# Kernel tuning notes

Hardware: AMD Instinct MI355X
Metric: run time of the kernel (lower is better)

## Reference

```python
import jax, jax.numpy as jnp
import numpy as np

T, B, D, H, F, E = 2048, 2, 1024, 16, 4096, 8
HD = D // H
EPS = 1.1920929e-07  # torch.finfo(float32).eps


def setup_inputs() -> dict:
    key = jax.random.key(0)
    ks = jax.random.split(key, 20)
    sc = D ** -0.5
    n = lambda k, shape, s: jax.random.normal(k, shape, jnp.float32) * s
    return {
        "x": jax.random.normal(ks[0], (T, B, D), jnp.float32),
        "Wq": n(ks[1], (D, D), sc), "bq": jnp.zeros((D,), jnp.float32),
        "Wk": n(ks[2], (D, D), sc), "bk": jnp.zeros((D,), jnp.float32),
        "Wv": n(ks[3], (D, D), sc), "bv": jnp.zeros((D,), jnp.float32),
        "Wo": n(ks[4], (D, D), sc), "bo": jnp.zeros((D,), jnp.float32),
        "ln1_g": jnp.ones((D,), jnp.float32), "ln1_b": jnp.zeros((D,), jnp.float32),
        "ln2_g": jnp.ones((D,), jnp.float32), "ln2_b": jnp.zeros((D,), jnp.float32),
        "wg": n(ks[5], (D, E), sc),
        "W1": n(ks[6], (E, D, F), sc), "b1": jnp.zeros((E, F), jnp.float32),
        "W2": n(ks[7], (E, F, D), F ** -0.5), "b2": jnp.zeros((E, D), jnp.float32),
    }


def layer_norm(x, g, b):
    m = jnp.mean(x, -1, keepdims=True)
    v = jnp.var(x, -1, keepdims=True)
    return (x - m) * jax.lax.rsqrt(v + 1e-5) * g + b


def attention(x, Wq, bq, Wk, bk, Wv, bv, Wo, bo):
    t, b, d = x.shape
    q = ((x @ Wq + bq) * (HD ** -0.5)).reshape(t, b, H, HD)
    k = (x @ Wk + bk).reshape(t, b, H, HD)
    v = (x @ Wv + bv).reshape(t, b, H, HD)
    a = jax.nn.softmax(jnp.einsum('tbhd,sbhd->bhts', q, k), axis=-1)
    o = jnp.einsum('bhts,sbhd->tbhd', a, v).reshape(t, b, d)
    return o @ Wo + bo


def moe(xf, wg, W1, b1, W2, b2):
    # xf: [S, D] tokens (batch-major order, matching x.transpose(0,1).reshape(-1,d))
    S = xf.shape[0]
    C = 2 * ((S + E - 1) // E)  # fairseq top2 train capacity
    logits = xf.astype(jnp.float32) @ wg.astype(jnp.float32)
    gates = jax.nn.softmax(logits, axis=-1)
    idx1 = jnp.argmax(gates, axis=-1)
    m1 = jax.nn.one_hot(idx1, E, dtype=jnp.int32)
    idx2 = jnp.argmax(jnp.where(m1 > 0, -jnp.inf, logits), axis=-1)
    m2 = jax.nn.one_hot(idx2, E, dtype=jnp.int32)
    g1 = jnp.take_along_axis(gates, idx1[:, None], 1)[:, 0]
    g2 = jnp.take_along_axis(gates, idx2[:, None], 1)[:, 0]
    loc1 = jnp.cumsum(m1, axis=0) - 1
    loc2 = jnp.cumsum(m2, axis=0) - 1 + jnp.sum(m1, axis=0, keepdims=True)
    pos1 = jnp.sum(loc1 * m1, axis=1)
    pos2 = jnp.sum(loc2 * m2, axis=1)
    l_aux = jnp.mean(jnp.mean(gates, 0) * jnp.mean(m1.astype(jnp.float32), 0)) * E * E
    k1 = (pos1 < C).astype(xf.dtype)
    k2 = (pos2 < C).astype(xf.dtype)
    g1 = g1.astype(xf.dtype) * k1
    g2 = g2.astype(xf.dtype) * k2
    den = jnp.maximum(g1 + g2, EPS)
    g1, g2 = g1 / den, g2 / den
    f1 = idx1 * C + jnp.minimum(pos1, C - 1)
    f2 = idx2 * C + jnp.minimum(pos2, C - 1)
    # dispatch (unweighted, capacity-masked)
    buf = jnp.zeros((E * C, D), xf.dtype)
    buf = buf.at[f1].add(xf * k1[:, None]).at[f2].add(xf * k2[:, None])
    h = jax.nn.relu(jnp.einsum('ecd,edf->ecf', buf.reshape(E, C, D), W1) + b1[:, None, :])
    out = (jnp.einsum('ecf,efd->ecd', h, W2) + b2[:, None, :]).reshape(E * C, D)
    # combine with normalized gates (dropped tokens have zero gate)
    y = g1[:, None] * out[f1] + g2[:, None] * out[f2]
    return y, l_aux


def reference(x, Wq, bq, Wk, bk, Wv, bv, Wo, bo, ln1_g, ln1_b, ln2_g, ln2_b, wg, W1, b1, W2, b2):
    # pre-LN self-attention block
    residual = x
    h = layer_norm(x, ln1_g, ln1_b)
    h = attention(h, Wq, bq, Wk, bk, Wv, bv, Wo, bo)
    x = residual + h
    # pre-LN MoE FFN block
    residual = x
    h = layer_norm(x, ln2_g, ln2_b)
    hb = jnp.swapaxes(h, 0, 1).reshape(-1, D)  # [B*T, D]
    y, l_aux = moe(hb, wg, W1, b1, W2, b2)
    y = jnp.swapaxes(y.reshape(B, T, D), 0, 1)
    x = residual + y
    return x, l_aux
```

## Files before the change

kernel.cpp:

```cpp
#include <hip/hip_runtime.h>

#define TT 2048
#define BB 2
#define DD 1024
#define HH 16
#define HD 64
#define FF 4096
#define EE 8
#define SS (TT*BB)
#define CAP 1024
#define EPSF 1.1920929e-07f

typedef __attribute__((ext_vector_type(8))) short short8;
typedef __attribute__((ext_vector_type(4))) float floatx4;

static __device__ inline unsigned short f2bf(float f){
    unsigned int u = __float_as_uint(f);
    unsigned int r = (u + 0x7fffu + ((u>>16)&1u)) >> 16;
    return (unsigned short)r;
}
static __device__ inline float bf2f(unsigned short h){
    return __uint_as_float(((unsigned int)h)<<16);
}
static __device__ inline void split2(float x, unsigned short& h, unsigned short& l){
    unsigned short hh = f2bf(x);
    h = hh;
    l = f2bf(x - bf2f(hh));
}
static __device__ inline void split2t(float x, unsigned short& h, unsigned short& l){
    unsigned int u = __float_as_uint(x);
    unsigned int hu = u & 0xffff0000u;
    h = (unsigned short)(hu>>16);
    float r = x - __uint_as_float(hu);
    l = (unsigned short)(__float_as_uint(r)>>16);
}
#define GETF4(v,j) ((j)==0?(v).x:(j)==1?(v).y:(j)==2?(v).z:(v).w)
#define GETU4(v,j) ((j)==0?(v).x:(j)==1?(v).y:(j)==2?(v).z:(v).w)

__global__ __launch_bounds__(256) void ln_kernel(const float* __restrict__ x,
    const float* __restrict__ gam, const float* __restrict__ bet, float* __restrict__ o)
{
    int row = blockIdx.x;
    int tid = threadIdx.x;
    float4 v = ((const float4*)(x + (size_t)row*DD))[tid];
    float s  = v.x+v.y+v.z+v.w;
    float ss = v.x*v.x+v.y*v.y+v.z*v.z+v.w*v.w;
    __shared__ float r1[256], r2[256];
    r1[tid]=s; r2[tid]=ss;
    __syncthreads();
    for (int off=128; off>0; off>>=1){
        if (tid<off){ r1[tid]+=r1[tid+off]; r2[tid]+=r2[tid+off]; }
        __syncthreads();
    }
    float mean = r1[0] * (1.f/DD);
    float var  = r2[0] * (1.f/DD) - mean*mean;
    float inv  = 1.f / sqrtf(var + 1e-5f);
    float4 g = ((const float4*)gam)[tid];
    float4 b = ((const float4*)bet)[tid];
    float4 r;
    r.x = (v.x-mean)*inv*g.x + b.x;
    r.y = (v.y-mean)*inv*g.y + b.y;
    r.z = (v.z-mean)*inv*g.z + b.z;
    r.w = (v.w-mean)*inv*g.w + b.w;
    ((float4*)(o + (size_t)row*DD))[tid] = r;
}

__global__ __launch_bounds__(256) void ln_split_kernel(const float* __restrict__ x,
    const float* __restrict__ gam, const float* __restrict__ bet,
    unsigned short* __restrict__ oh, unsigned short* __restrict__ ol)
{
    int row = blockIdx.x;
    int tid = threadIdx.x;
    float4 v = ((const float4*)(x + (size_t)row*DD))[tid];
    float s  = v.x+v.y+v.z+v.w;
    float ss = v.x*v.x+v.y*v.y+v.z*v.z+v.w*v.w;
    __shared__ float r1[256], r2[256];
    r1[tid]=s; r2[tid]=ss;
    __syncthreads();
    for (int off=128; off>0; off>>=1){
        if (tid<off){ r1[tid]+=r1[tid+off]; r2[tid]+=r2[tid+off]; }
        __syncthreads();
    }
    float mean = r1[0] * (1.f/DD);
    float var  = r2[0] * (1.f/DD) - mean*mean;
    float inv  = 1.f / sqrtf(var + 1e-5f);
    float4 g = ((const float4*)gam)[tid];
    float4 b = ((const float4*)bet)[tid];
    float4 r;
    r.x = (v.x-mean)*inv*g.x + b.x;
    r.y = (v.y-mean)*inv*g.y + b.y;
    r.z = (v.z-mean)*inv*g.z + b.z;
    r.w = (v.w-mean)*inv*g.w + b.w;
    ushort4 hv, lv;
    split2(r.x, hv.x, lv.x);
    split2(r.y, hv.y, lv.y);
    split2(r.z, hv.z, lv.z);
    split2(r.w, hv.w, lv.w);
    ((ushort4*)(oh + (size_t)row*DD))[tid] = hv;
    ((ushort4*)(ol + (size_t)row*DD))[tid] = lv;
}

template<bool RELU, bool OUTBF16>
__global__ __launch_bounds__(256) void gemm_mfma(
    const unsigned short* __restrict__ A, const unsigned short* __restrict__ Bt,
    const float* __restrict__ bias, float* __restrict__ Cf,
    unsigned short* __restrict__ Cb,
    int M, int N, int K, long wStride, int bStride, int rowsPerExp)
{
    __shared__ unsigned short As[128*64];
    __shared__ unsigned short Bs[128*64];
    const int tid = threadIdx.x, lane = tid&63;
    const int w = tid>>6, wr = w>>1, wc = w&1;
    const int m0 = blockIdx.y*128, n0 = blockIdx.x*128;
    const int e = m0 / rowsPerExp;
    const unsigned short* Bp = Bt + (size_t)e*wStride;
    const int srow = tid>>3, sslot = tid&7;
    floatx4 zf = {0.f,0.f,0.f,0.f};
    floatx4 acc[4][4];
    #pragma unroll
    for (int m=0;m<4;m++)
        #pragma unroll
        for (int n=0;n<4;n++) acc[m][n]=zf;

    short8 ar[4], br[4];
    #pragma unroll
    for (int i=0;i<4;i++){
        int r = srow + i*32;
        ar[i] = *(const short8*)(A  + (size_t)(m0+r)*K + sslot*8);
        br[i] = *(const short8*)(Bp + (size_t)(n0+r)*K + sslot*8);
    }
    const int NT = K/64;
    for (int kt=0; kt<NT; kt++){
        __syncthreads();
        #pragma unroll
        for (int i=0;i<4;i++){
            int r = srow + i*32;
            int off = r*64 + ((sslot ^ (r&7))<<3);
            *(short8*)(&As[off]) = ar[i];
            *(short8*)(&Bs[off]) = br[i];
        }
        __syncthreads();
        if (kt+1 < NT){
            int k0 = (kt+1)*64;
            #pragma unroll
            for (int i=0;i<4;i++){
                int r = srow + i*32;
                ar[i] = *(const short8*)(A  + (size_t)(m0+r)*K + k0 + sslot*8);
                br[i] = *(const short8*)(Bp + (size_t)(n0+r)*K + k0 + sslot*8);
            }
        }
        #pragma unroll
        for (int kk=0;kk<2;kk++){
            short8 af[4], bf[4];
            int kgrp = kk*4 + (lane>>4);
            #pragma unroll
            for (int m=0;m<4;m++){
                int rowa = wr*64 + m*16 + (lane&15);
                af[m] = *(const short8*)(&As[rowa*64 + ((kgrp ^ (rowa&7))<<3)]);
                int rowb = wc*64 + m*16 + (lane&15);
                bf[m] = *(const short8*)(&Bs[rowb*64 + ((kgrp ^ (rowb&7))<<3)]);
            }
            #pragma unroll
            for (int m=0;m<4;m++)
                #pragma unroll
                for (int n=0;n<4;n++)
                    acc[m][n] = __builtin_amdgcn_mfma_f32_16x16x32_bf16(af[m], bf[n], acc[m][n], 0,0,0);
        }
    }
    int colg = n0 + wc*64 + (lane&15);
    int rowg = m0 + wr*64 + ((lane>>4)<<2);
    #pragma unroll
    for (int n=0;n<4;n++){
        float bv = bias[e*bStride + colg + n*16];
        #pragma unroll
        for (int m=0;m<4;m++){
            #pragma unroll
            for (int i2=0;i2<4;i2++){
                float v = acc[m][n][i2] + bv;
                if (RELU) v = fmaxf(v, 0.f);
                size_t o = (size_t)(rowg + m*16 + i2)*N + colg + n*16;
                if (OUTBF16) Cb[o] = f2bf(v); else Cf[o] = v;
            }
        }
    }
}

template<bool QKV>
__global__ __launch_bounds__(256) void gemm_mfma_s(
    const unsigned short* __restrict__ Ahi, const unsigned short* __restrict__ Alo,
    const unsigned short* __restrict__ Bhi, const unsigned short* __restrict__ Blo,
    const float* __restrict__ b0, const float* __restrict__ b1p, const float* __restrict__ b2p,
    const float* __restrict__ res,
    float* __restrict__ o0,
    unsigned short* __restrict__ kh, unsigned short* __restrict__ kl,
    unsigned short* __restrict__ vh, unsigned short* __restrict__ vl,
    int M, int K)
{
    __shared__ unsigned short As[128*64];
    __shared__ unsigned short Bs[128*64];
    const int tid = threadIdx.x, lane = tid&63;
    const int w = tid>>6, wr = w>>1, wc = w&1;
    const int m0 = blockIdx.y*128, n0 = blockIdx.x*128;
    const int row = tid>>1, khalf = tid&1;
    floatx4 zf = {0.f,0.f,0.f,0.f};
    floatx4 acc[4][4];
    #pragma unroll
    for (int m=0;m<4;m++)
        #pragma unroll
        for (int n=0;n<4;n++) acc[m][n]=zf;

    short8 awh0,awh1,awl0,awl1, bwh0,bwh1,bwl0,bwl1;
    {
        size_t ao = (size_t)(m0+row)*K + khalf*16;
        awh0 = *(const short8*)(Ahi+ao); awh1 = *(const short8*)(Ahi+ao+8);
        awl0 = *(const short8*)(Alo+ao); awl1 = *(const short8*)(Alo+ao+8);
        size_t bo = (size_t)(n0+row)*K + khalf*16;
        bwh0 = *(const short8*)(Bhi+bo); bwh1 = *(const short8*)(Bhi+bo+8);
        bwl0 = *(const short8*)(Blo+bo); bwl1 = *(const short8*)(Blo+bo+8);
    }
    const int NT = K/32;
    for (int kt=0; kt<NT; kt++){
        __syncthreads();
        {
            int base = row*64, sw = row&7;
            int g0 = khalf*2, g1 = khalf*2+1;
            *(short8*)(&As[base + ((g0^sw)<<3)])     = awh0;
            *(short8*)(&As[base + ((g1^sw)<<3)])     = awh1;
            *(short8*)(&As[base + (((g0+4)^sw)<<3)]) = awl0;
            *(short8*)(&As[base + (((g1+4)^sw)<<3)]) = awl1;
            *(short8*)(&Bs[base + ((g0^sw)<<3)])     = bwh0;
            *(short8*)(&Bs[base + ((g1^sw)<<3)])     = bwh1;
            *(short8*)(&Bs[base + (((g0+4)^sw)<<3)]) = bwl0;
            *(short8*)(&Bs[base + (((g1+4)^sw)<<3)]) = bwl1;
        }
        __syncthreads();
        if (kt+1 < NT){
            int k0 = (kt+1)*32;
            size_t ao = (size_t)(m0+row)*K + k0 + khalf*16;
            awh0 = *(const short8*)(Ahi+ao); awh1 = *(const short8*)(Ahi+ao+8);
            awl0 = *(const short8*)(Alo+ao); awl1 = *(const short8*)(Alo+ao+8);
            size_t bo = (size_t)(n0+row)*K + k0 + khalf*16;
            bwh0 = *(const short8*)(Bhi+bo); bwh1 = *(const short8*)(Bhi+bo+8);
            bwl0 = *(const short8*)(Blo+bo); bwl1 = *(const short8*)(Blo+bo+8);
        }
        {
            int kg = lane>>4;
            short8 afh[4], afl[4], bfh[4], bfl[4];
            #pragma unroll
            for (int m=0;m<4;m++){
                int ra = wr*64 + m*16 + (lane&15);
                afh[m] = *(const short8*)(&As[ra*64 + ((kg ^ (ra&7))<<3)]);
                afl[m] = *(const short8*)(&As[ra*64 + (((kg+4) ^ (ra&7))<<3)]);
                int rb = wc*64 + m*16 + (lane&15);
                bfh[m] = *(const short8*)(&Bs[rb*64 + ((kg ^ (rb&7))<<3)]);
                bfl[m] = *(const short8*)(&Bs[rb*64 + (((kg+4) ^ (rb&7))<<3)]);
            }
            #pragma unroll
            for (int m=0;m<4;m++)
                #pragma unroll
                for (int n=0;n<4;n++){
                    acc[m][n] = __builtin_amdgcn_mfma_f32_16x16x32_bf16(afl[m], bfh[n], acc[m][n], 0,0,0);
                    acc[m][n] = __builtin_amdgcn_mfma_f32_16x16x32_bf16(afh[m], bfl[n], acc[m][n], 0,0,0);
                    acc[m][n] = __builtin_amdgcn_mfma_f32_16x16x32_bf16(afh[m], bfh[n], acc[m][n], 0,0,0);
                }
        }
    }
    int colg = n0 + wc*64 + (lane&15);
    int rowg = m0 + wr*64 + ((lane>>4)<<2);
    if (QKV){
        int chunk = n0>>10;
        int colc = colg & 1023;
        const float* bp = chunk==0 ? b0 : (chunk==1 ? b1p : b2p);
        #pragma unroll
        for (int n=0;n<4;n++){
            float bv = bp[colc + n*16];
            #pragma unroll
            for (int m=0;m<4;m++){
                #pragma unroll
                for (int i2=0;i2<4;i2++){
                    int r = rowg + m*16 + i2;
                    float v = acc[m][n][i2] + bv;
                    size_t off = (size_t)r*DD + colc + n*16;
                    if (chunk==0){
                        o0[off] = v*0.125f;
                    } else {
                        unsigned short hh, ll;
                        split2(v, hh, ll);
                        if (chunk==1){ kh[off]=hh; kl[off]=ll; }
                        else         { vh[off]=hh; vl[off]=ll; }
                    }
                }
            }
        }
    } else {
        #pragma unroll
        for (int n=0;n<4;n++){
            float bv = b0[colg + n*16];
            #pragma unroll
            for (int m=0;m<4;m++){
                #pragma unroll
                for (int i2=0;i2<4;i2++){
                    int r = rowg + m*16 + i2;
                    float v = acc[m][n][i2] + bv + res[(size_t)r*DD + colg + n*16];
                    o0[(size_t)r*DD + colg + n*16] = v;
                }
            }
        }
    }
}

__global__ __launch_bounds__(256) void attn_mfma(const float* __restrict__ q,
    const unsigned short* __restrict__ khi, const unsigned short* __restrict__ klo,
    const unsigned short* __restrict__ vhi, const unsigned short* __restrict__ vlo,
    unsigned short* __restrict__ ohi, unsigned short* __restrict__ olo)
{
    __shared__ unsigned short Kh[64*64], Kl[64*64];
    __shared__ unsigned short Vh[64*64], Vl[64*64];
    __shared__ unsigned short Ph[4*16*64];
    const int tid = threadIdx.x, lane = tid&63, w = tid>>6;
    const int t0 = blockIdx.x*64;
    const int b = blockIdx.y>>4, h = blockIdx.y&15;

    short8 qh[2], ql[2];
    #pragma unroll
    for (int kk=0;kk<2;kk++){
        const float* qp = q + ((size_t)(t0 + 16*w + (lane&15))*BB + b)*DD + h*64 + kk*32 + (lane>>4)*8;
        float4 f0 = ((const float4*)qp)[0];
        float4 f1 = ((const float4*)qp)[1];
        unsigned short hh[8], ll[8];
        #pragma unroll
        for (int j=0;j<4;j++){ split2(GETF4(f0,j), hh[j], ll[j]); }
        #pragma unroll
        for (int j=0;j<4;j++){ split2(GETF4(f1,j), hh[4+j], ll[4+j]); }
        qh[kk] = *(short8*)hh; ql[kk] = *(short8*)ll;
    }

    const int kr = tid>>2, kq = tid&3;
    const int vs0 = (tid&15)*4, vd0 = (tid>>4)*4;
    short8 kwh0,kwh1,kwl0,kwl1;
    ushort4 vwh[4], vwl[4];
    {
        const unsigned short* kp = khi + ((size_t)kr*BB + b)*DD + h*64 + kq*16;
        const unsigned short* lp = klo + ((size_t)kr*BB + b)*DD + h*64 + kq*16;
        kwh0 = *(const short8*)(kp); kwh1 = *(const short8*)(kp+8);
        kwl0 = *(const short8*)(lp); kwl1 = *(const short8*)(lp+8);
        #pragma unroll
        for (int i=0;i<4;i++){
            size_t vo = ((size_t)(vs0+i)*BB + b)*DD + h*64 + vd0;
            vwh[i] = *(const ushort4*)(vhi + vo);
            vwl[i] = *(const ushort4*)(vlo + vo);
        }
    }

    float m_st[4] = {-3.0e38f,-3.0e38f,-3.0e38f,-3.0e38f};
    float l_st[4] = {0.f,0.f,0.f,0.f};
    floatx4 zf = {0.f,0.f,0.f,0.f};
    floatx4 oacc[4];
    #pragma unroll
    for (int n=0;n<4;n++) oacc[n]=zf;

    for (int s0=0; s0<TT; s0+=64){
        __syncthreads();
        {
            int base = kr*64, sw = kr&7;
            int g0 = kq*2, g1 = kq*2+1;
            *(short8*)(&Kh[base + ((g0^sw)<<3)]) = kwh0;
            *(short8*)(&Kh[base + ((g1^sw)<<3)]) = kwh1;
            *(short8*)(&Kl[base + ((g0^sw)<<3)]) = kwl0;
            *(short8*)(&Kl[base + ((g1^sw)<<3)]) = kwl1;
        }
        {
            int g = vs0>>3, so = vs0&7;
            #pragma unroll
            for (int j=0;j<4;j++){
                int d = vd0 + j;
                ushort4 hv, lv;
                hv.x=GETU4(vwh[0],j); hv.y=GETU4(vwh[1],j); hv.z=GETU4(vwh[2],j); hv.w=GETU4(vwh[3],j);
                lv.x=GETU4(vwl[0],j); lv.y=GETU4(vwl[1],j); lv.z=GETU4(vwl[2],j); lv.w=GETU4(vwl[3],j);
                int off = d*64 + ((g ^ (d&7))<<3) + so;
                *(ushort4*)(&Vh[off]) = hv;
                *(ushort4*)(&Vl[off]) = lv;
            }
        }
        __syncthreads();
        if (s0+64 < TT){
            const unsigned short* kp = khi + ((size_t)(s0+64+kr)*BB + b)*DD + h*64 + kq*16;
            const unsigned short* lp = klo + ((size_t)(s0+64+kr)*BB + b)*DD + h*64 + kq*16;
            kwh0 = *(const short8*)(kp); kwh1 = *(const short8*)(kp+8);
            kwl0 = *(const short8*)(lp); kwl1 = *(const short8*)(lp+8);
            #pragma unroll
            for (int i=0;i<4;i++){
                size_t vo = ((size_t)(s0+64+vs0+i)*BB + b)*DD + h*64 + vd0;
                vwh[i] = *(const ushort4*)(vhi + vo);
                vwl[i] = *(const ushort4*)(vlo + vo);
            }
        }
        floatx4 sacc[4];
        __builtin_amdgcn_s_setprio(1);
        #pragma unroll
        for (int n=0;n<4;n++){
            floatx4 s = zf;
            #pragma unroll
            for (int kk=0;kk<2;kk++){
                int g = kk*4 + (lane>>4);
                int rb = n*16 + (lane&15);
                short8 kbh = *(const short8*)(&Kh[rb*64 + ((g ^ (rb&7))<<3)]);
                short8 kbl = *(const short8*)(&Kl[rb*64 + ((g ^ (rb&7))<<3)]);
                s = __builtin_amdgcn_mfma_f32_16x16x32_bf16(ql[kk], kbh, s, 0,0,0);
                s = __builtin_amdgcn_mfma_f32_16x16x32_bf16(qh[kk], kbl, s, 0,0,0);
                s = __builtin_amdgcn_mfma_f32_16x16x32_bf16(qh[kk], kbh, s, 0,0,0);
            }
            sacc[n] = s;
        }
        __builtin_amdgcn_s_setprio(0);
        float mx[4];
        #pragma unroll
        for (int r=0;r<4;r++)
            mx[r] = fmaxf(fmaxf(sacc[0][r], sacc[1][r]), fmaxf(sacc[2][r], sacc[3][r]));
        #pragma unroll
        for (int sh=1; sh<16; sh<<=1){
            #pragma unroll
            for (int r=0;r<4;r++) mx[r] = fmaxf(mx[r], __shfl_xor(mx[r], sh));
        }
        float corr[4];
        #pragma unroll
        for (int r=0;r<4;r++){
            float nm = fmaxf(m_st[r], mx[r]);
            corr[r] = __expf(m_st[r] - nm);
            m_st[r] = nm;
        }
        float ts[4] = {0.f,0.f,0.f,0.f};
        #pragma unroll
        for (int n=0;n<4;n++){
            #pragma unroll
            for (int r=0;r<4;r++){
                float p = __expf(sacc[n][r] - m_st[r]);
                ts[r] += p;
                int q2 = ((lane>>4)<<2) + r;
                int s2 = n*16 + (lane&15);
                int off = w*1024 + q2*64 + (((s2>>3) ^ (q2&7))<<3) + (s2&7);
                Ph[off] = f2bf(p);
            }
        }
        #pragma unroll
        for (int sh=1; sh<16; sh<<=1){
            #pragma unroll
            for (int r=0;r<4;r++) ts[r] += __shfl_xor(ts[r], sh);
        }
        #pragma unroll
        for (int r=0;r<4;r++) l_st[r] = l_st[r]*corr[r] + ts[r];
        #pragma unroll
        for (int n=0;n<4;n++)
            #pragma unroll
            for (int r=0;r<4;r++) oacc[n][r] *= corr[r];
        __builtin_amdgcn_s_setprio(1);
        #pragma unroll
        for (int kk=0;kk<2;kk++){
            int g = kk*4 + (lane>>4);
            int rq = lane&15;
            short8 pa = *(const short8*)(&Ph[w*1024 + rq*64 + ((g ^ (rq&7))<<3)]);
            #pragma unroll
            for (int n=0;n<4;n++){
                int rd = n*16 + (lane&15);
                short8 vbh = *(const short8*)(&Vh[rd*64 + ((g ^ (rd&7))<<3)]);
                short8 vbl = *(const short8*)(&Vl[rd*64 + ((g ^ (rd&7))<<3)]);
                oacc[n] = __builtin_amdgcn_mfma_f32_16x16x32_bf16(pa, vbl, oacc[n], 0,0,0);
                oacc[n] = __builtin_amdgcn_mfma_f32_16x16x32_bf16(pa, vbh, oacc[n], 0,0,0);
            }
        }
        __builtin_amdgcn_s_setprio(0);
    }
    float il[4];
    #pragma unroll
    for (int r=0;r<4;r++) il[r] = 1.f/l_st[r];
    int qrow = t0 + 16*w + ((lane>>4)<<2);
    #pragma unroll
    for (int n=0;n<4;n++){
        #pragma unroll
        for (int r=0;r<4;r++){
            float v = oacc[n][r]*il[r];
            unsigned short hh, ll;
            split2(v, hh, ll);
            size_t off = ((size_t)(qrow+r)*BB + b)*DD + h*64 + n*16 + (lane&15);
            ohi[off] = hh; olo[off] = ll;
        }
    }
}

__global__ __launch_bounds__(256) void transpose_bf16_k(const float* __restrict__ in,
    unsigned short* __restrict__ outp, int R, int C)
{
    __shared__ float t[64][65];
    int e = blockIdx.z;
    const float* ip = in + (size_t)e*R*C;
    unsigned short* op = outp + (size_t)e*R*C;
    int r0 = blockIdx.y*64, c0 = blockIdx.x*64;
    int tid = threadIdx.x;
    #pragma unroll
    for (int i=0;i<4;i++){
        int ch = i*256 + tid;
        int r = ch>>4, c4 = (ch&15)*4;
        float4 v = *(const float4*)(ip + (size_t)(r0+r)*C + c0 + c4);
        t[r][c4+0]=v.x; t[r][c4+1]=v.y; t[r][c4+2]=v.z; t[r][c4+3]=v.w;
    }
    __syncthreads();
    #pragma unroll
    for (int i=0;i<4;i++){
        int ch = i*256 + tid;
        int rr = ch>>4, c4 = (ch&15)*4;
        ushort4 o;
        o.x = f2bf(t[c4+0][rr]); o.y = f2bf(t[c4+1][rr]);
        o.z = f2bf(t[c4+2][rr]); o.w = f2bf(t[c4+3][rr]);
        *(ushort4*)(op + (size_t)(c0+rr)*R + r0 + c4) = o;
    }
}

__global__ __launch_bounds__(256) void transpose_split_k(const float* __restrict__ in,
    unsigned short* __restrict__ oh, unsigned short* __restrict__ ol, int R, int C)
{
    __shared__ float t[64][65];
    int r0 = blockIdx.y*64, c0 = blockIdx.x*64;
    int tid = threadIdx.x;
    #pragma unroll
    for (int i=0;i<4;i++){
        int ch = i*256 + tid;
        int r = ch>>4, c4 = (ch&15)*4;
        float4 v = *(const float4*)(in + (size_t)(r0+r)*C + c0 + c4);
        t[r][c4+0]=v.x; t[r][c4+1]=v.y; t[r][c4+2]=v.z; t[r][c4+3]=v.w;
    }
    __syncthreads();
    #pragma unroll
    for (int i=0;i<4;i++){
        int ch = i*256 + tid;
        int rr = ch>>4, c4 = (ch&15)*4;
        ushort4 hv, lv;
        split2(t[c4+0][rr], hv.x, lv.x);
        split2(t[c4+1][rr], hv.y, lv.y);
        split2(t[c4+2][rr], hv.z, lv.z);
        split2(t[c4+3][rr], hv.w, lv.w);
        size_t off = (size_t)(c0+rr)*R + r0 + c4;
        *(ushort4*)(oh + off) = hv;
        *(ushort4*)(ol + off) = lv;
    }
}

__global__ __launch_bounds__(256) void gather_bf16_k(const float* __restrict__ h2,
    const int* __restrict__ s2r, unsigned short* __restrict__ buf)
{
    int s = blockIdx.x; int row = s2r[s]; int c = threadIdx.x;
    float4 v = make_float4(0.f,0.f,0.f,0.f);
    if (row>=0) v = *(const float4*)(h2 + (size_t)row*DD + c*4);
    ushort4 o;
    o.x=f2bf(v.x); o.y=f2bf(v.y); o.z=f2bf(v.z); o.w=f2bf(v.w);
    *(ushort4*)(buf + (size_t)s*DD + c*4) = o;
}

__global__ __launch_bounds__(256) void route_kernel(const float* __restrict__ h2,
    const float* __restrict__ wgm, float* __restrict__ gates,
    int* __restrict__ idx1, int* __restrict__ idx2,
    float* __restrict__ g1, float* __restrict__ g2)
{
    int wid = threadIdx.x >> 6, lane = threadIdx.x & 63;
    int s = blockIdx.x*4 + wid;
    int row = (s % TT)*BB + (s / TT);
    const float* hr = h2 + (size_t)row*DD;
    float acc[EE] = {};
    #pragma unroll
    for (int c=0;c<16;c++){
        int d = c*64 + lane;
        float xv = hr[d];
        const float* wr = wgm + (size_t)d*EE;
        #pragma unroll
        for (int e2=0;e2<EE;e2++) acc[e2] += xv * wr[e2];
    }
    #pragma unroll
    for (int off=32; off>0; off>>=1){
        #pragma unroll
        for (int e2=0;e2<EE;e2++) acc[e2] += __shfl_down(acc[e2], off);
    }
    if (lane==0){
        float mx = acc[0];
        #pragma unroll
        for (int e2=1;e2<EE;e2++) mx = fmaxf(mx, acc[e2]);
        float ex[EE]; float sum=0.f;
        #pragma unroll
        for (int e2=0;e2<EE;e2++){ ex[e2] = __expf(acc[e2]-mx); sum += ex[e2]; }
        float inv = 1.f/sum;
        int i1=0; float bv1=acc[0];
        #pragma unroll
        for (int e2=1;e2<EE;e2++){ if (acc[e2] > bv1){ bv1=acc[e2]; i1=e2; } }
        int i2=-1; float bv2=-3.0e38f;
        #pragma unroll
        for (int e2=0;e2<EE;e2++){ if (e2!=i1 && acc[e2] > bv2){ bv2=acc[e2]; i2=e2; } }
        #pragma unroll
        for (int e2=0;e2<EE;e2++) gates[(size_t)s*EE + e2] = ex[e2]*inv;
        idx1[s]=i1; idx2[s]=i2;
        g1[s]=ex[i1]*inv; g2[s]=ex[i2]*inv;
    }
}

__global__ __launch_bounds__(256) void scan_kernel(
    const float* __restrict__ gates, const int* __restrict__ idx1, const int* __restrict__ idx2,
    const float* __restrict__ g1, const float* __restrict__ g2,
    float* __restrict__ g1n, float* __restrict__ g2n,
    int* __restrict__ f1, int* __restrict__ f2, int* __restrict__ slot2row,
    float* __restrict__ laux)
{
    __shared__ int i1s[SS];
    __shared__ int i2s[SS];
    __shared__ int cnt1[256][EE];
    __shared__ int cnt2[256][EE];
    __shared__ float gsum[256][EE];
    __shared__ int tot1[EE];
    int tid = threadIdx.x;
    for (int i=tid;i<EE*CAP;i+=256) slot2row[i] = -1;
    for (int i=tid;i<SS;i+=256){ i1s[i]=idx1[i]; i2s[i]=idx2[i]; }
    __syncthreads();
    int c1l[EE]={}, c2l[EE]={};
    float gl[EE]={};
    int base = tid*16;
    for (int qq=0;qq<16;qq++){
        int s = base+qq;
        c1l[i1s[s]]++; c2l[i2s[s]]++;
        #pragma unroll
        for (int e2=0;e2<EE;e2++) gl[e2] += gates[(size_t)s*EE+e2];
    }
    #pragma unroll
    for (int e2=0;e2<EE;e2++){ cnt1[tid][e2]=c1l[e2]; cnt2[tid][e2]=c2l[e2]; gsum[tid][e2]=gl[e2]; }
    __syncthreads();
    if (tid < EE){
        int e2 = tid;
        int run=0;
        for (int t=0;t<256;t++){ int tmp=cnt1[t][e2]; cnt1[t][e2]=run; run+=tmp; }
        tot1[e2]=run;
        run=0;
        for (int t=0;t<256;t++){ int tmp=cnt2[t][e2]; cnt2[t][e2]=run; run+=tmp; }
        float gr=0.f;
        for (int t=0;t<256;t++) gr += gsum[t][e2];
        gsum[0][e2]=gr;
    }
    __syncthreads();
    int p1[EE], p2[EE];
    #pragma unroll
    for (int e2=0;e2<EE;e2++){ p1[e2]=cnt1[tid][e2]; p2[e2]=cnt2[tid][e2]+tot1[e2]; }
    for (int qq=0;qq<16;qq++){
        int s = base+qq;
        int e1 = i1s[s], e2v = i2s[s];
        int pos1 = p1[e1]++;
        int pos2 = p2[e2v]++;
        float gv1 = g1[s], gv2 = g2[s];
        float gm1 = (pos1<CAP)? gv1 : 0.f;
        float gm2 = (pos2<CAP)? gv2 : 0.f;
        float den = fmaxf(gm1+gm2, EPSF);
        g1n[s] = gm1/den; g2n[s] = gm2/den;
        int ff1 = e1*CAP + (pos1<CAP?pos1:CAP-1);
        int ff2 = e2v*CAP + (pos2<CAP?pos2:CAP-1);
        f1[s]=ff1; f2[s]=ff2;
        int hrow = (s % TT)*BB + (s / TT);
        if (pos1<CAP) slot2row[ff1]=hrow;
        if (pos2<CAP) slot2row[ff2]=hrow;
    }
    if (tid==0){
        float a=0.f;
        #pragma unroll
        for (int e2=0;e2<EE;e2++) a += (gsum[0][e2]*(1.f/SS)) * ((float)tot1[e2]*(1.f/SS));
        laux[0] = a * (float)EE;
    }
}

__global__ __launch_bounds__(256) void combine_kernel(const float* __restrict__ x2,
    const float* __restrict__ eout, const float* __restrict__ g1n, const float* __restrict__ g2n,
    const int* __restrict__ f1, const int* __restrict__ f2, float* __restrict__ out)
{
    int s = blockIdx.x;
    float a = g1n[s], b = g2n[s];
    int s1 = f1[s], s2 = f2[s];
    int row = (s % TT)*BB + (s / TT);
    int c = threadIdx.x;
    float4 o1 = ((const float4*)(eout + (size_t)s1*DD))[c];
    float4 o2 = ((const float4*)(eout + (size_t)s2*DD))[c];
    float4 xr = ((const float4*)(x2 + (size_t)row*DD))[c];
    float4 r;
    r.x = xr.x + a*o1.x + b*o2.x;
    r.y = xr.y + a*o1.y + b*o2.y;
    r.z = xr.z + a*o1.z + b*o2.z;
    r.w = xr.w + a*o1.w + b*o2.w;
    ((float4*)(out + (size_t)row*DD))[c] = r;
}

extern "C" void kernel_launch(void* const* d_in, const int* in_sizes, int n_in,
                              void* d_out, int out_size, void* d_ws, size_t ws_size,
                              hipStream_t stream)
{
    const float* x    = (const float*)d_in[0];
    const float* Wq   = (const float*)d_in[1];
    const float* bq   = (const float*)d_in[2];
    const float* Wk   = (const float*)d_in[3];
    const float* bk   = (const float*)d_in[4];
    const float* Wv   = (const float*)d_in[5];
    const float* bv   = (const float*)d_in[6];
    const float* Wo   = (const float*)d_in[7];
    const float* bo   = (const float*)d_in[8];
    const float* ln1g = (const float*)d_in[9];
    const float* ln1b = (const float*)d_in[10];
    const float* ln2g = (const float*)d_in[11];
    const float* ln2b = (const float*)d_in[12];
    const float* wgm  = (const float*)d_in[13];
    const float* W1   = (const float*)d_in[14];
    const float* b1   = (const float*)d_in[15];
    const float* W2   = (const float*)d_in[16];
    const float* b2   = (const float*)d_in[17];
    float* out = (float*)d_out;

    char* w = (char*)d_ws;
    unsigned short* h1hi = (unsigned short*)(w);
    unsigned short* h1lo = (unsigned short*)(w + ((size_t)8<<20));
    float*          qb   = (float*)(w + ((size_t)16<<20));
    unsigned short* Khg  = (unsigned short*)(w + ((size_t)32<<20));
    unsigned short* Klg  = (unsigned short*)(w + ((size_t)40<<20));
    unsigned short* Vhg  = (unsigned short*)(w + ((size_t)48<<20));
    unsigned short* Vlg  = (unsigned short*)(w + ((size_t)56<<20));
    float*          x2   = (float*)(w + ((size_t)64<<20));
    unsigned short* bufb = (unsigned short*)(w + ((size_t)80<<20));
    unsigned short* hb   = (unsigned short*)(w + ((size_t)96<<20));
    unsigned short* Bqkv_hi = (unsigned short*)(w + ((size_t)96<<20));
    unsigned short* Bqkv_lo = (unsigned short*)(w + ((size_t)102<<20));
    unsigned short* Bo_hi   = (unsigned short*)(w + ((size_t)108<<20));
    unsigned short* Bo_lo   = (unsigned short*)(w + ((size_t)110<<20));
    unsigned short* W1t  = (unsigned short*)(w + ((size_t)160<<20));
    unsigned short* W2t  = (unsigned short*)(w + ((size_t)224<<20));
    float*          ffno = (float*)(w + ((size_t)32<<20));
    char*  sm   = w + ((size_t)288<<20);
    float* gates   = (float*)(sm);                sm += (size_t)SS*EE*4;
    int*   idx1    = (int*)(sm);                  sm += SS*4;
    int*   idx2    = (int*)(sm);                  sm += SS*4;
    float* g1      = (float*)(sm);                sm += SS*4;
    float* g2      = (float*)(sm);                sm += SS*4;
    float* g1n     = (float*)(sm);                sm += SS*4;
    float* g2n     = (float*)(sm);                sm += SS*4;
    int*   f1      = (int*)(sm);                  sm += SS*4;
    int*   f2      = (int*)(sm);                  sm += SS*4;
    int*   slot2row= (int*)(sm);                  sm += EE*CAP*4;

    transpose_bf16_k<<<dim3(FF/64, DD/64, EE), 256, 0, stream>>>(W1, W1t, DD, FF);
    transpose_bf16_k<<<dim3(DD/64, FF/64, EE), 256, 0, stream>>>(W2, W2t, FF, DD);
    transpose_split_k<<<dim3(16,16), 256, 0, stream>>>(Wq, Bqkv_hi,                   Bqkv_lo,                   DD, DD);
    transpose_split_k<<<dim3(16,16), 256, 0, stream>>>(Wk, Bqkv_hi + (size_t)DD*DD,   Bqkv_lo + (size_t)DD*DD,   DD, DD);
    transpose_split_k<<<dim3(16,16), 256, 0, stream>>>(Wv, Bqkv_hi + (size_t)2*DD*DD, Bqkv_lo + (size_t)2*DD*DD, DD, DD);
    transpose_split_k<<<dim3(16,16), 256, 0, stream>>>(Wo, Bo_hi, Bo_lo, DD, DD);
    ln_split_kernel<<<SS, 256, 0, stream>>>(x, ln1g, ln1b, h1hi, h1lo);
    gemm_mfma_s<true><<<dim3(24, SS/128), 256, 0, stream>>>(
        h1hi, h1lo, Bqkv_hi, Bqkv_lo, bq, bk, bv, nullptr, qb, Khg, Klg, Vhg, Vlg, SS, DD);
    attn_mfma<<<dim3(TT/64, BB*HH), 256, 0, stream>>>(qb, Khg, Klg, Vhg, Vlg, h1hi, h1lo);
    gemm_mfma_s<false><<<dim3(8, SS/128), 256, 0, stream>>>(
        h1hi, h1lo, Bo_hi, Bo_lo, bo, bo, bo, x, x2, nullptr, nullptr, nullptr, nullptr, SS, DD);
    ln_kernel<<<SS, 256, 0, stream>>>(x2, ln2g, ln2b, qb);
    route_kernel<<<SS/4, 256, 0, stream>>>(qb, wgm, gates, idx1, idx2, g1, g2);
    scan_kernel<<<1, 256, 0, stream>>>(gates, idx1, idx2, g1, g2,
        g1n, g2n, f1, f2, slot2row, out + (size_t)SS*DD);
    gather_bf16_k<<<EE*CAP, 256, 0, stream>>>(qb, slot2row, bufb);
    gemm_mfma<true,true><<<dim3(FF/128, (EE*CAP)/128), 256, 0, stream>>>(
        bufb, W1t, b1, nullptr, hb, EE*CAP, FF, DD, (long)FF*DD, FF, CAP);
    gemm_mfma<false,false><<<dim3(DD/128, (EE*CAP)/128), 256, 0, stream>>>(
        hb, W2t, b2, ffno, nullptr, EE*CAP, DD, FF, (long)DD*FF, DD, CAP);
    combine_kernel<<<SS, 256, 0, stream>>>(x2, ffno, g1n, g2n, f1, f2, out);
    (void)in_sizes; (void)n_in; (void)out_size; (void)ws_size;
}
```

Baseline: 673.0 us.

## Double attention query tile to 128 rows with 512-thread blocks sharing K/V tiles

The attention kernel now processes 128 query rows per block with 8 waves instead of 64 rows with 4 waves. Each K/V tile staged in shared memory is reused by twice as many queries, which halves global K/V traffic. The cooperative load mapping is reworked so each of the 512 threads loads half as much. The trade-off is half as many blocks (512) on the GPU and larger per-block shared memory for P, which may reduce occupancy and parallelism.

```diff
diff --git a/kernel.cpp b/kernel.cpp
--- a/kernel.cpp
+++ b/kernel.cpp
@@ -26,13 +26,6 @@
     unsigned short hh = f2bf(x);
     h = hh;
     l = f2bf(x - bf2f(hh));
-}
-static __device__ inline void split2t(float x, unsigned short& h, unsigned short& l){
-    unsigned int u = __float_as_uint(x);
-    unsigned int hu = u & 0xffff0000u;
-    h = (unsigned short)(hu>>16);
-    float r = x - __uint_as_float(hu);
-    l = (unsigned short)(__float_as_uint(r)>>16);
 }
 #define GETF4(v,j) ((j)==0?(v).x:(j)==1?(v).y:(j)==2?(v).z:(v).w)
 #define GETU4(v,j) ((j)==0?(v).x:(j)==1?(v).y:(j)==2?(v).z:(v).w)
@@ -309,16 +302,16 @@
     }
 }
 
-__global__ __launch_bounds__(256) void attn_mfma(const float* __restrict__ q,
+__global__ __launch_bounds__(512) void attn_mfma(const float* __restrict__ q,
     const unsigned short* __restrict__ khi, const unsigned short* __restrict__ klo,
     const unsigned short* __restrict__ vhi, const unsigned short* __restrict__ vlo,
     unsigned short* __restrict__ ohi, unsigned short* __restrict__ olo)
 {
     __shared__ unsigned short Kh[64*64], Kl[64*64];
     __shared__ unsigned short Vh[64*64], Vl[64*64];
-    __shared__ unsigned short Ph[4*16*64];
+    __shared__ unsigned short Ph[8*16*64];
     const int tid = threadIdx.x, lane = tid&63, w = tid>>6;
-    const int t0 = blockIdx.x*64;
+    const int t0 = blockIdx.x*128;
     const int b = blockIdx.y>>4, h = blockIdx.y&15;
 
     short8 qh[2], ql[2];
@@ -335,17 +328,16 @@
         qh[kk] = *(short8*)hh; ql[kk] = *(short8*)ll;
     }
 
-    const int kr = tid>>2, kq = tid&3;
-    const int vs0 = (tid&15)*4, vd0 = (tid>>4)*4;
-    short8 kwh0,kwh1,kwl0,kwl1;
-    ushort4 vwh[4], vwl[4];
+    const int kr = tid>>3, kq = tid&7;
+    const int vs0 = (tid&31)*2, vd0 = (tid>>5)*4;
+    short8 kwh, kwl;
+    ushort4 vwh[2], vwl[2];
     {
-        const unsigned short* kp = khi + ((size_t)kr*BB + b)*DD + h*64 + kq*16;
-        const unsigned short* lp = klo + ((size_t)kr*BB + b)*DD + h*64 + kq*16;
-        kwh0 = *(const short8*)(kp); kwh1 = *(const short8*)(kp+8);
-        kwl0 = *(const short8*)(lp); kwl1 = *(const short8*)(lp+8);
-        #pragma unroll
-        for (int i=0;i<4;i++){
+        size_t ko = ((size_t)kr*BB + b)*DD + h*64 + kq*8;
+        kwh = *(const short8*)(khi + ko);
+        kwl = *(const short8*)(klo + ko);
+        #pragma unroll
+        for (int i=0;i<2;i++){
             size_t vo = ((size_t)(vs0+i)*BB + b)*DD + h*64 + vd0;
             vwh[i] = *(const ushort4*)(vhi + vo);
             vwl[i] = *(const ushort4*)(vlo + vo);
@@ -362,34 +354,30 @@
     for (int s0=0; s0<TT; s0+=64){
         __syncthreads();
         {
-            int base = kr*64, sw = kr&7;
-            int g0 = kq*2, g1 = kq*2+1;
-            *(short8*)(&Kh[base + ((g0^sw)<<3)]) = kwh0;
-            *(short8*)(&Kh[base + ((g1^sw)<<3)]) = kwh1;
-            *(short8*)(&Kl[base + ((g0^sw)<<3)]) = kwl0;
-            *(short8*)(&Kl[base + ((g1^sw)<<3)]) = kwl1;
+            int off = kr*64 + ((kq ^ (kr&7))<<3);
+            *(short8*)(&Kh[off]) = kwh;
+            *(short8*)(&Kl[off]) = kwl;
         }
         {
             int g = vs0>>3, so = vs0&7;
             #pragma unroll
             for (int j=0;j<4;j++){
                 int d = vd0 + j;
-                ushort4 hv, lv;
-                hv.x=GETU4(vwh[0],j); hv.y=GETU4(vwh[1],j); hv.z=GETU4(vwh[2],j); hv.w=GETU4(vwh[3],j);
-                lv.x=GETU4(vwl[0],j); lv.y=GETU4(vwl[1],j); lv.z=GETU4(vwl[2],j); lv.w=GETU4(vwl[3],j);
+                ushort2 hv, lv;
+                hv.x=GETU4(vwh[0],j); hv.y=GETU4(vwh[1],j);
+                lv.x=GETU4(vwl[0],j); lv.y=GETU4(vwl[1],j);
                 int off = d*64 + ((g ^ (d&7))<<3) + so;
-                *(ushort4*)(&Vh[off]) = hv;
-                *(ushort4*)(&Vl[off]) = lv;
+                *(ushort2*)(&Vh[off]) = hv;
+                *(ushort2*)(&Vl[off]) = lv;
             }
         }
         __syncthreads();
         if (s0+64 < TT){
-            const unsigned short* kp = khi + ((size_t)(s0+64+kr)*BB + b)*DD + h*64 + kq*16;
-            const unsigned short* lp = klo + ((size_t)(s0+64+kr)*BB + b)*DD + h*64 + kq*16;
-            kwh0 = *(const short8*)(kp); kwh1 = *(const short8*)(kp+8);
-            kwl0 = *(const short8*)(lp); kwl1 = *(const short8*)(lp+8);
-            #pragma unroll
-            for (int i=0;i<4;i++){
+            size_t ko = ((size_t)(s0+64+kr)*BB + b)*DD + h*64 + kq*8;
+            kwh = *(const short8*)(khi + ko);
+            kwl = *(const short8*)(klo + ko);
+            #pragma unroll
+            for (int i=0;i<2;i++){
                 size_t vo = ((size_t)(s0+64+vs0+i)*BB + b)*DD + h*64 + vd0;
                 vwh[i] = *(const ushort4*)(vhi + vo);
                 vwl[i] = *(const ushort4*)(vlo + vo);
@@ -751,7 +739,7 @@
     ln_split_kernel<<<SS, 256, 0, stream>>>(x, ln1g, ln1b, h1hi, h1lo);
     gemm_mfma_s<true><<<dim3(24, SS/128), 256, 0, stream>>>(
         h1hi, h1lo, Bqkv_hi, Bqkv_lo, bq, bk, bv, nullptr, qb, Khg, Klg, Vhg, Vlg, SS, DD);
-    attn_mfma<<<dim3(TT/64, BB*HH), 256, 0, stream>>>(qb, Khg, Klg, Vhg, Vlg, h1hi, h1lo);
+    attn_mfma<<<dim3(TT/128, BB*HH), 512, 0, stream>>>(qb, Khg, Klg, Vhg, Vlg, h1hi, h1lo);
     gemm_mfma_s<false><<<dim3(8, SS/128), 256, 0, stream>>>(
         h1hi, h1lo, Bo_hi, Bo_lo, bo, bo, bo, x, x2, nullptr, nullptr, nullptr, nullptr, SS, DD);
     ln_kernel<<<SS, 256, 0, stream>>>(x2, ln2g, ln2b, qb);
```

Result: no change. 666.5 us (-1.0%).
